# Kernel optimization log

Hardware: AMD Instinct MI355X
Metric: run time of the kernel (lower is better)

## Reference

```python
import jax, jax.numpy as jnp
import numpy as np

DIMS = 2048
HEADS = 16
HEAD_DIM = DIMS // HEADS  # 128
WIN = 256
THETA = 10000.0


def rotate_half(x):
    x1, x2 = jnp.split(x, 2, axis=-1)
    return jnp.concatenate([-x2, x1], axis=-1)


def rope_freqs(seq_len):
    inv_freq = 1.0 / (THETA ** (jnp.arange(0, HEAD_DIM, 2, dtype=jnp.float32) / HEAD_DIM))
    f = jnp.outer(jnp.arange(seq_len, dtype=jnp.float32), inv_freq)  # [S, D/2]
    return jnp.concatenate([f, f], axis=-1)[None, :, None, :]  # [1, S, 1, D]


def setup_inputs() -> dict:
    key = jax.random.key(0)
    ks = jax.random.split(key, 5)
    B, S = 2, 8192
    scale = 1.0 / np.sqrt(DIMS).astype(np.float32)
    return {
        "hidden_states": jax.random.normal(ks[0], (B, S, DIMS), jnp.float32),
        "Wq": jax.random.normal(ks[1], (DIMS, DIMS), jnp.float32) * scale,
        "Wk": jax.random.normal(ks[2], (DIMS, DIMS), jnp.float32) * scale,
        "Wv": jax.random.normal(ks[3], (DIMS, DIMS), jnp.float32) * scale,
        "Wo": jax.random.normal(ks[4], (DIMS, DIMS), jnp.float32) * scale,
    }


def reference(hidden_states, Wq, Wk, Wv, Wo):
    B, S, _ = hidden_states.shape
    # projections (weights stored [in, out])
    q = (hidden_states @ Wq).reshape(B, S, HEADS, HEAD_DIM)
    k = (hidden_states @ Wk).reshape(B, S, HEADS, HEAD_DIM)
    v = (hidden_states @ Wv).reshape(B, S, HEADS, HEAD_DIM)

    freqs = rope_freqs(S)
    cos, sin = jnp.cos(freqs), jnp.sin(freqs)
    q = q * cos + rotate_half(q) * sin
    k = k * cos + rotate_half(k) * sin

    C = S // WIN
    qc = q.reshape(B, C, WIN, HEADS, HEAD_DIM)
    kc = k.reshape(B, C, WIN, HEADS, HEAD_DIM)
    vc = v.reshape(B, C, WIN, HEADS, HEAD_DIM)

    # previous chunk's K/V (zeros for chunk 0; masked out anyway)
    kp = jnp.concatenate([jnp.zeros_like(kc[:, :1]), kc[:, :-1]], axis=1)
    vp = jnp.concatenate([jnp.zeros_like(vc[:, :1]), vc[:, :-1]], axis=1)
    kcat = jnp.concatenate([kp, kc], axis=2)  # [B, C, 2W, H, D]
    vcat = jnp.concatenate([vp, vc], axis=2)

    scores = jnp.einsum('bcqhd,bckhd->bchqk', qc, kcat) / np.float32(np.sqrt(HEAD_DIM))

    causal = jnp.tril(jnp.ones((WIN, WIN), dtype=bool))  # current-chunk causal
    prev_ok = (jnp.arange(C) > 0)[:, None, None]  # chunk 0 has no previous chunk
    mask = jnp.concatenate([
        jnp.broadcast_to(prev_ok, (C, WIN, WIN)),
        jnp.broadcast_to(causal[None], (C, WIN, WIN)),
    ], axis=-1)  # [C, W, 2W]

    scores = jnp.where(mask[None, :, None], scores, -jnp.inf)
    probs = jax.nn.softmax(scores, axis=-1)
    out = jnp.einsum('bchqk,bckhd->bcqhd', probs, vcat)
    out = out.reshape(B, S, DIMS)
    return out @ Wo
```

## Files before the change

kernel.cpp:

```cpp
#include <hip/hip_runtime.h>
#include <cmath>

#define DIMS 2048
#define SEQ  8192
#define NB   2
#define HEADS 16
#define HD   128
#define WINW 256
#define MROWS 16384
#define NCH  32

using bf16x8 = __attribute__((ext_vector_type(8))) short;
using f32x4  = __attribute__((ext_vector_type(4))) float;

__device__ __forceinline__ unsigned short f2bf(float f) {
  unsigned int u = __float_as_uint(f);
  u += 0x7FFF + ((u >> 16) & 1);
  return (unsigned short)(u >> 16);
}

__device__ __forceinline__ void async16(const unsigned short* g, unsigned short* l) {
  __builtin_amdgcn_global_load_lds((const __attribute__((address_space(1))) void*)g,
                                   (__attribute__((address_space(3))) void*)l,
                                   16, 0, 0);
}

#define BAR() __builtin_amdgcn_s_barrier()
#define WAIT_LGKM0() do { asm volatile("s_waitcnt lgkmcnt(0)" ::: "memory"); \
                          __builtin_amdgcn_sched_barrier(0); } while (0)
#define WAIT_LGKM(n) do { asm volatile("s_waitcnt lgkmcnt(" #n ")" ::: "memory"); \
                          __builtin_amdgcn_sched_barrier(0); } while (0)
#define ORDER() asm volatile("" ::: "memory")
#define WAIT_VM(n) asm volatile("s_waitcnt vmcnt(" #n ")" ::: "memory")
#define MFMA16(a, b, c) __builtin_amdgcn_mfma_f32_16x16x32_bf16(a, b, c, 0, 0, 0)

__global__ __launch_bounds__(256) void prep(
    const float* __restrict__ w0, const float* __restrict__ w1,
    const float* __restrict__ w2, const float* __restrict__ w3,
    const float* __restrict__ H,
    unsigned short* __restrict__ Wt, unsigned short* __restrict__ Hb,
    float* __restrict__ cosT, float* __restrict__ sinT) {
  __shared__ unsigned short tile[64][65];
  const int bid = blockIdx.x;
  const int t = threadIdx.x;
  if (bid < 4096) {
    const int z = bid & 3;
    const int rest = bid >> 2;
    const int n0 = (rest & 31) * 64, k0 = (rest >> 5) * 64;
    const float* W = (z == 0) ? w0 : (z == 1) ? w1 : (z == 2) ? w2 : w3;
    unsigned short* O = Wt + (size_t)z * DIMS * DIMS;
    #pragma unroll
    for (int p = 0; p < 16; ++p) {
      int i = p * 4 + (t >> 6);
      int j = t & 63;
      tile[i][j] = f2bf(W[(size_t)(k0 + i) * DIMS + n0 + j]);
    }
    __syncthreads();
    #pragma unroll
    for (int p = 0; p < 16; ++p) {
      int a = p * 4 + (t >> 6);
      int b = t & 63;
      O[(size_t)(n0 + a) * DIMS + k0 + b] = tile[b][a];
    }
  } else if (bid < 6144) {
    const long n4 = (long)MROWS * DIMS / 4;
    long i = (long)(bid - 4096) * 256 + t;
    for (; i < n4; i += 524288) {
      float4 v = ((const float4*)H)[i];
      ushort4 o;
      o.x = f2bf(v.x); o.y = f2bf(v.y); o.z = f2bf(v.z); o.w = f2bf(v.w);
      ((ushort4*)Hb)[i] = o;
    }
  } else {
    int tl = (bid - 6144) * 256 + t;
    int pos = tl >> 6, i = tl & 63;
    double inv = pow(10000.0, -(double)i / 64.0);
    double ang = (double)pos * inv;
    cosT[tl] = (float)cos(ang);
    sinT[tl] = (float)sin(ang);
  }
}

template<int MODE>
__global__ __launch_bounds__(512, 2) void gemm256(
    const unsigned short* __restrict__ A,
    const unsigned short* __restrict__ WtAll,
    unsigned short* __restrict__ OutB,
    float* __restrict__ OutF,
    const float* __restrict__ cosT,
    const float* __restrict__ sinT) {
  __shared__ __align__(1024) unsigned short lds[65536];
  unsigned short* const As0 = lds;
  unsigned short* const Bs0 = lds + 16384;
  unsigned short* const As1 = lds + 32768;
  unsigned short* const Bs1 = lds + 49152;

  const int tid = threadIdx.x;
  const int wid = tid >> 6, lane = tid & 63;
  const int lo = lane & 15, hi = lane >> 4;
  const int wm = wid >> 2, wn = wid & 3;
  const int flip = (lo & 7) << 4;

  const int nwg = gridDim.x;
  const int orig = blockIdx.x;
  const int bid = (orig & 7) * (nwg >> 3) + (orig >> 3);

  int by, bx, z;
  if (MODE == 0) {
    z = bid >> 9;
    by = (bid & 511) >> 3;
    bx = bid & 7;
  } else {
    by = bid >> 3; bx = bid & 7; z = 3;
  }
  const int m0 = by * 256, n0 = bx * 256;
  const unsigned short* const Ag = A;
  const unsigned short* const Bg = WtAll + (size_t)z * DIMS * DIMS;

  f32x4 acc[8][4];
  #pragma unroll
  for (int i = 0; i < 8; ++i)
    #pragma unroll
    for (int j = 0; j < 4; ++j)
      acc[i][j] = (f32x4){0.f, 0.f, 0.f, 0.f};

  auto stage_half = [&](const unsigned short* __restrict__ G, int grow0, int tile,
                        unsigned short* dst) {
    const int k0 = tile * 64;
    #pragma unroll
    for (int h8 = 0; h8 < 2; ++h8) {
      const int c = h8 * 8 + wid;
      const int row = c * 8 + (lane >> 3);
      const int col8 = (lane & 7) ^ (lane >> 3);
      async16(G + (size_t)(grow0 + row) * DIMS + k0 + col8 * 8, dst + c * 512);
    }
  };
  auto rdA = [&](const unsigned short* base, int i, int kk) -> bf16x8 {
    const int r = i * 32 + wm * 16 + lo;
    const int cb = (kk * 64 + hi * 16) ^ flip;
    return *(const bf16x8*)((const char*)base + r * 128 + cb);
  };
  auto rdB = [&](const unsigned short* base, int j, int kk) -> bf16x8 {
    const int r = j * 64 + wn * 16 + lo;
    const int cb = (kk * 64 + hi * 16) ^ flip;
    return *(const bf16x8*)((const char*)base + r * 128 + cb);
  };

  bf16x8 aq[4][2], b0[2][2], b1[2][2];

  stage_half(Ag, m0,       0, As0);
  stage_half(Bg, n0,       0, Bs0);
  stage_half(Ag, m0 + 128, 0, As0 + 8192);
  stage_half(Bg, n0 + 128, 0, Bs0 + 8192);
  stage_half(Ag, m0,       1, As1);
  stage_half(Bg, n0,       1, Bs1);
  stage_half(Bg, n0 + 128, 1, Bs1 + 8192);
  WAIT_VM(6);
  BAR();

  #pragma unroll 1
  for (int it = 0; it < 16; ++it) {
    const int t = 2 * it;
    const bool pre = (it < 15);
    #pragma unroll
    for (int i = 0; i < 4; ++i) aq[i][0] = rdA(As0, i, 0);
    #pragma unroll
    for (int j = 0; j < 2; ++j) b0[j][0] = rdB(Bs0, j, 0);
    ORDER();
    #pragma unroll
    for (int i = 0; i < 4; ++i) aq[i][1] = rdA(As0, i, 1);
    #pragma unroll
    for (int j = 0; j < 2; ++j) b0[j][1] = rdB(Bs0, j, 1);
    stage_half(Ag, m0 + 128, t + 1, As1 + 8192);
    WAIT_LGKM(6);
    __builtin_amdgcn_s_setprio(1);
    #pragma unroll
    for (int i = 0; i < 4; ++i)
      #pragma unroll
      for (int j = 0; j < 2; ++j)
        acc[i][j] = MFMA16(aq[i][0], b0[j][0], acc[i][j]);
    WAIT_LGKM0();
    #pragma unroll
    for (int i = 0; i < 4; ++i)
      #pragma unroll
      for (int j = 0; j < 2; ++j)
        acc[i][j] = MFMA16(aq[i][1], b0[j][1], acc[i][j]);
    __builtin_amdgcn_s_setprio(0);
    BAR();
    #pragma unroll
    for (int j = 0; j < 2; ++j) b1[j][0] = rdB(Bs0, 2 + j, 0);
    ORDER();
    #pragma unroll
    for (int j = 0; j < 2; ++j) b1[j][1] = rdB(Bs0, 2 + j, 1);
    if (pre) stage_half(Ag, m0, t + 2, As0);
    WAIT_LGKM(2);
    __builtin_amdgcn_s_setprio(1);
    #pragma unroll
    for (int i = 0; i < 4; ++i)
      #pragma unroll
      for (int j = 0; j < 2; ++j)
        acc[i][2 + j] = MFMA16(aq[i][0], b1[j][0], acc[i][2 + j]);
    WAIT_LGKM0();
    #pragma unroll
    for (int i = 0; i < 4; ++i)
      #pragma unroll
      for (int j = 0; j < 2; ++j)
        acc[i][2 + j] = MFMA16(aq[i][1], b1[j][1], acc[i][2 + j]);
    __builtin_amdgcn_s_setprio(0);
    BAR();
    #pragma unroll
    for (int i = 0; i < 4; ++i) aq[i][0] = rdA(As0, 4 + i, 0);
    ORDER();
    #pragma unroll
    for (int i = 0; i < 4; ++i) aq[i][1] = rdA(As0, 4 + i, 1);
    if (pre) stage_half(Bg, n0, t + 2, Bs0);
    WAIT_LGKM(4);
    __builtin_amdgcn_s_setprio(1);
    #pragma unroll
    for (int i = 0; i < 4; ++i)
      #pragma unroll
      for (int j = 0; j < 2; ++j)
        acc[4 + i][j] = MFMA16(aq[i][0], b0[j][0], acc[4 + i][j]);
    WAIT_LGKM0();
    #pragma unroll
    for (int i = 0; i < 4; ++i)
      #pragma unroll
      for (int j = 0; j < 2; ++j)
        acc[4 + i][j] = MFMA16(aq[i][1], b0[j][1], acc[4 + i][j]);
    __builtin_amdgcn_s_setprio(0);
    BAR();
    if (pre) stage_half(Bg, n0 + 128, t + 2, Bs0 + 8192);
    __builtin_amdgcn_s_setprio(1);
    #pragma unroll
    for (int kk = 0; kk < 2; ++kk)
      #pragma unroll
      for (int i = 0; i < 4; ++i)
        #pragma unroll
        for (int j = 0; j < 2; ++j)
          acc[4 + i][2 + j] = MFMA16(aq[i][kk], b1[j][kk], acc[4 + i][2 + j]);
    __builtin_amdgcn_s_setprio(0);
    if (it == 15) { WAIT_VM(0); } else { WAIT_VM(6); }
    BAR();
    #pragma unroll
    for (int i = 0; i < 4; ++i) aq[i][0] = rdA(As1, i, 0);
    #pragma unroll
    for (int j = 0; j < 2; ++j) b0[j][0] = rdB(Bs1, j, 0);
    ORDER();
    #pragma unroll
    for (int i = 0; i < 4; ++i) aq[i][1] = rdA(As1, i, 1);
    #pragma unroll
    for (int j = 0; j < 2; ++j) b0[j][1] = rdB(Bs1, j, 1);
    if (pre) stage_half(Ag, m0 + 128, t + 2, As0 + 8192);
    WAIT_LGKM(6);
    __builtin_amdgcn_s_setprio(1);
    #pragma unroll
    for (int i = 0; i < 4; ++i)
      #pragma unroll
      for (int j = 0; j < 2; ++j)
        acc[i][j] = MFMA16(aq[i][0], b0[j][0], acc[i][j]);
    WAIT_LGKM0();
    #pragma unroll
    for (int i = 0; i < 4; ++i)
      #pragma unroll
      for (int j = 0; j < 2; ++j)
        acc[i][j] = MFMA16(aq[i][1], b0[j][1], acc[i][j]);
    __builtin_amdgcn_s_setprio(0);
    BAR();
    #pragma unroll
    for (int j = 0; j < 2; ++j) b1[j][0] = rdB(Bs1, 2 + j, 0);
    ORDER();
    #pragma unroll
    for (int j = 0; j < 2; ++j) b1[j][1] = rdB(Bs1, 2 + j, 1);
    if (pre) stage_half(Ag, m0, t + 3, As1);
    WAIT_LGKM(2);
    __builtin_amdgcn_s_setprio(1);
    #pragma unroll
    for (int i = 0; i < 4; ++i)
      #pragma unroll
      for (int j = 0; j < 2; ++j)
        acc[i][2 + j] = MFMA16(aq[i][0], b1[j][0], acc[i][2 + j]);
    WAIT_LGKM0();
    #pragma unroll
    for (int i = 0; i < 4; ++i)
      #pragma unroll
      for (int j = 0; j < 2; ++j)
        acc[i][2 + j] = MFMA16(aq[i][1], b1[j][1], acc[i][2 + j]);
    __builtin_amdgcn_s_setprio(0);
    BAR();
    #pragma unroll
    for (int i = 0; i < 4; ++i) aq[i][0] = rdA(As1, 4 + i, 0);
    ORDER();
    #pragma unroll
    for (int i = 0; i < 4; ++i) aq[i][1] = rdA(As1, 4 + i, 1);
    if (pre) stage_half(Bg, n0, t + 3, Bs1);
    WAIT_LGKM(4);
    __builtin_amdgcn_s_setprio(1);
    #pragma unroll
    for (int i = 0; i < 4; ++i)
      #pragma unroll
      for (int j = 0; j < 2; ++j)
        acc[4 + i][j] = MFMA16(aq[i][0], b0[j][0], acc[4 + i][j]);
    WAIT_LGKM0();
    #pragma unroll
    for (int i = 0; i < 4; ++i)
      #pragma unroll
      for (int j = 0; j < 2; ++j)
        acc[4 + i][j] = MFMA16(aq[i][1], b0[j][1], acc[4 + i][j]);
    __builtin_amdgcn_s_setprio(0);
    BAR();
    if (pre) stage_half(Bg, n0 + 128, t + 3, Bs1 + 8192);
    __builtin_amdgcn_s_setprio(1);
    #pragma unroll
    for (int kk = 0; kk < 2; ++kk)
      #pragma unroll
      for (int i = 0; i < 4; ++i)
        #pragma unroll
        for (int j = 0; j < 2; ++j)
          acc[4 + i][2 + j] = MFMA16(aq[i][kk], b1[j][kk], acc[4 + i][2 + j]);
    __builtin_amdgcn_s_setprio(0);
    WAIT_VM(6);
    BAR();
  }

  if (MODE == 0 && z == 2) {
    unsigned short* vt = OutB + (size_t)2 * MROWS * DIMS;
    #pragma unroll
    for (int i = 0; i < 8; ++i) {
      const int row0 = m0 + i * 32 + wm * 16 + hi * 4;
      const int bb = row0 >> 13;
      const int s0 = row0 & (SEQ - 1);
      #pragma unroll
      for (int j = 0; j < 4; ++j) {
        const int colg = n0 + j * 64 + wn * 16 + lo;
        ushort4 pk;
        pk.x = f2bf(acc[i][j][0]); pk.y = f2bf(acc[i][j][1]);
        pk.z = f2bf(acc[i][j][2]); pk.w = f2bf(acc[i][j][3]);
        *(ushort4*)&vt[(((size_t)(bb * 2048 + colg)) << 13) + s0] = pk;
      }
    }
  } else {
    unsigned short* outb = (MODE == 0) ? (OutB + (size_t)z * MROWS * DIMS)
                                       : (unsigned short*)nullptr;
    #pragma unroll
    for (int i = 0; i < 8; ++i) {
      #pragma unroll
      for (int rr = 0; rr < 4; ++rr) {
        const int row = m0 + i * 32 + wm * 16 + hi * 4 + rr;
        const int s = row & (SEQ - 1);
        if (MODE == 1) {
          float* o = OutF + (size_t)row * DIMS + n0;
          #pragma unroll
          for (int j = 0; j < 4; ++j) o[j * 64 + wn * 16 + lo] = acc[i][j][rr];
        } else {
          unsigned short* o = outb + (size_t)row * DIMS + n0;
          const int d = wn * 16 + lo;
          const float cc = cosT[s * 64 + d], sn = sinT[s * 64 + d];
          #pragma unroll
          for (int p = 0; p < 2; ++p) {
            const float v1 = acc[i][2 * p][rr], v2 = acc[i][2 * p + 1][rr];
            o[p * 128 + d]      = f2bf(v1 * cc - v2 * sn);
            o[p * 128 + d + 64] = f2bf(v2 * cc + v1 * sn);
          }
        }
      }
    }
  }
}

__global__ __launch_bounds__(256, 2) void attn(
    const unsigned short* __restrict__ Qb,
    const unsigned short* __restrict__ Kb,
    const unsigned short* __restrict__ Vt,
    unsigned short* __restrict__ AO) {
  __shared__ unsigned short Ksm[2][64 * 128];
  __shared__ unsigned short Vsm[2][128 * 64];
  __shared__ unsigned short Psm[4 * 32 * 64];

  const int nwg = gridDim.x;
  const int orig = blockIdx.x;
  const int bid = (orig & 7) * (nwg >> 3) + (orig >> 3);

  const int qh = bid & 1;
  const int h = (bid >> 1) & 15;
  const int c = (bid >> 5) & 31;
  const int b = bid >> 10;
  const int tid = threadIdx.x;
  const int wid = tid >> 6, lane = tid & 63;
  const int lo = lane & 15, hi = lane >> 4;
  const float SCALE = 0.08838834764831845f;

  const int qbase = qh * 128 + wid * 32;

  bf16x8 qf[2][4];
  {
    const size_t base = ((size_t)(b * SEQ + c * WINW + qbase + lo)) * DIMS + h * HD;
    #pragma unroll
    for (int m = 0; m < 2; ++m)
      #pragma unroll
      for (int ks = 0; ks < 4; ++ks)
        qf[m][ks] = *(const bf16x8*)&Qb[base + (size_t)m * 16 * DIMS + ks * 32 + hi * 8];
  }

  f32x4 O[2][8];
  float mrow[2][4], lrow[2][4];
  #pragma unroll
  for (int m = 0; m < 2; ++m) {
    #pragma unroll
    for (int n = 0; n < 8; ++n) O[m][n] = (f32x4){0.f, 0.f, 0.f, 0.f};
    #pragma unroll
    for (int r = 0; r < 4; ++r) { mrow[m][r] = -INFINITY; lrow[m][r] = 0.f; }
  }

  unsigned short* Pw = Psm + wid * 32 * 64;
  const int t0 = (c == 0) ? 4 : 0;
  const int tend = 5 + 2 * qh;

  const unsigned short* Kg0 = Kb + ((size_t)(b * SEQ + (c - 1) * WINW)) * DIMS + h * HD;
  const unsigned short* Vg0 = Vt + (((size_t)(b * 2048 + h * HD)) << 13) + (c - 1) * WINW;

  auto stageKV = [&](int t, int pb) {
    #pragma unroll
    for (int p = 0; p < 4; ++p) {
      const int cid = p * 256 + tid;
      const int row = cid >> 4, c16 = cid & 15;
      async16(Kg0 + (size_t)(t * 64 + row) * DIMS + ((c16 ^ (row & 7)) << 3),
              &Ksm[pb][cid * 8]);
    }
    #pragma unroll
    for (int p = 0; p < 4; ++p) {
      const int cid = p * 256 + tid;
      const int rd = cid >> 3, c8 = cid & 7;
      async16(Vg0 + ((size_t)rd << 13) + t * 64 + ((c8 ^ (rd & 7)) << 3),
              &Vsm[pb][cid * 8]);
    }
  };

  stageKV(t0, t0 & 1);
  for (int t = t0; t <= tend; ++t) {
    const int pb = t & 1;
    if (t < tend) { stageKV(t + 1, pb ^ 1); WAIT_VM(8); } else { WAIT_VM(0); }
    BAR();

    const bool active = (t < 4) || (((t - 4) << 6) <= qbase + 31);
    if (active) {
      f32x4 S[2][4];
      #pragma unroll
      for (int m = 0; m < 2; ++m)
        #pragma unroll
        for (int n = 0; n < 4; ++n)
          S[m][n] = (f32x4){0.f, 0.f, 0.f, 0.f};
      const char* Kbase = (const char*)&Ksm[pb][0];
      #pragma unroll
      for (int ks = 0; ks < 4; ++ks) {
        bf16x8 kf[4];
        #pragma unroll
        for (int n = 0; n < 4; ++n)
          kf[n] = *(const bf16x8*)(Kbase + (n * 16 + lo) * 256 +
                                   (((ks * 4 + hi) ^ (lo & 7)) << 4));
        #pragma unroll
        for (int m = 0; m < 2; ++m)
          #pragma unroll
          for (int n = 0; n < 4; ++n)
            S[m][n] = MFMA16(qf[m][ks], kf[n], S[m][n]);
      }

      float tmax[2][4];
      #pragma unroll
      for (int m = 0; m < 2; ++m) {
        #pragma unroll
        for (int r = 0; r < 4; ++r) {
          const int qrow = qbase + m * 16 + hi * 4 + r;
          float tm = -INFINITY;
          #pragma unroll
          for (int n = 0; n < 4; ++n) {
            const int kc = t * 64 + n * 16 + lo;
            float v = S[m][n][r] * SCALE;
            const bool ok = (kc < WINW) ? (c > 0) : ((kc - WINW) <= qrow);
            v = ok ? v : -INFINITY;
            S[m][n][r] = v;
            tm = fmaxf(tm, v);
          }
          tm = fmaxf(tm, __shfl_xor(tm, 1));
          tm = fmaxf(tm, __shfl_xor(tm, 2));
          tm = fmaxf(tm, __shfl_xor(tm, 4));
          tm = fmaxf(tm, __shfl_xor(tm, 8));
          tmax[m][r] = tm;
        }
      }
      float need = -INFINITY;
      #pragma unroll
      for (int m = 0; m < 2; ++m)
        #pragma unroll
        for (int r = 0; r < 4; ++r)
          need = fmaxf(need, tmax[m][r] - mrow[m][r]);
      const bool fast = __all(need <= 8.0f);

      #pragma unroll
      for (int m = 0; m < 2; ++m) {
        #pragma unroll
        for (int r = 0; r < 4; ++r) {
          float mused = mrow[m][r];
          if (!fast) {
            mused = fmaxf(mused, tmax[m][r]);
            const float corr = __expf(mrow[m][r] - mused);
            lrow[m][r] *= corr;
            #pragma unroll
            for (int n = 0; n < 8; ++n) O[m][n][r] *= corr;
            mrow[m][r] = mused;
          }
          float rsum = 0.f;
          #pragma unroll
          for (int n = 0; n < 4; ++n) {
            const float p = __expf(S[m][n][r] - mused);
            S[m][n][r] = p;
            rsum += p;
          }
          rsum += __shfl_xor(rsum, 1);
          rsum += __shfl_xor(rsum, 2);
          rsum += __shfl_xor(rsum, 4);
          rsum += __shfl_xor(rsum, 8);
          lrow[m][r] += rsum;
          const int q = m * 16 + hi * 4 + r;
          #pragma unroll
          for (int n = 0; n < 4; ++n) {
            const int boff = (q << 7) + (((n * 16 + lo) << 1) ^ ((q & 7) << 4));
            *(unsigned short*)((char*)Pw + boff) = f2bf(S[m][n][r]);
          }
        }
      }
      asm volatile("" ::: "memory");

      const char* Vbase = (const char*)&Vsm[pb][0];
      #pragma unroll
      for (int kk = 0; kk < 2; ++kk) {
        bf16x8 pf[2], vf[8];
        #pragma unroll
        for (int m = 0; m < 2; ++m) {
          const int q = m * 16 + lo;
          pf[m] = *(const bf16x8*)((const char*)Pw + (q << 7) +
                                   (((kk * 4 + hi) << 4) ^ ((q & 7) << 4)));
        }
        #pragma unroll
        for (int n = 0; n < 8; ++n)
          vf[n] = *(const bf16x8*)(Vbase + (n * 16 + lo) * 128 +
                                   (((kk * 4 + hi) ^ (lo & 7)) << 4));
        #pragma unroll
        for (int m = 0; m < 2; ++m)
          #pragma unroll
          for (int n = 0; n < 8; ++n)
            O[m][n] = MFMA16(pf[m], vf[n], O[m][n]);
      }
    }
    BAR();
  }

  #pragma unroll
  for (int m = 0; m < 2; ++m) {
    #pragma unroll
    for (int r = 0; r < 4; ++r) {
      const float inv = 1.f / lrow[m][r];
      const size_t row = (size_t)(b * SEQ + c * WINW + qbase + m * 16 + hi * 4 + r);
      unsigned short* o = AO + row * DIMS + h * HD;
      #pragma unroll
      for (int n = 0; n < 8; ++n)
        o[n * 16 + lo] = f2bf(O[m][n][r] * inv);
    }
  }
}

extern "C" void kernel_launch(void* const* d_in, const int* in_sizes, int n_in,
                              void* d_out, int out_size, void* d_ws, size_t ws_size,
                              hipStream_t stream) {
  const float* H  = (const float*)d_in[0];
  const float* Wq = (const float*)d_in[1];
  const float* Wk = (const float*)d_in[2];
  const float* Wv = (const float*)d_in[3];
  const float* Wo = (const float*)d_in[4];
  float* out = (float*)d_out;

  unsigned short* Wt  = (unsigned short*)d_ws;
  unsigned short* Hb  = Wt + (size_t)4 * DIMS * DIMS;
  unsigned short* QKV = Hb + (size_t)MROWS * DIMS;
  unsigned short* AO  = QKV + (size_t)3 * MROWS * DIMS;
  float* cosT = (float*)(AO + (size_t)MROWS * DIMS);
  float* sinT = cosT + (size_t)SEQ * 64;

  prep<<<8192, 256, 0, stream>>>(Wq, Wk, Wv, Wo, H, Wt, Hb, cosT, sinT);
  gemm256<0><<<1536, 512, 0, stream>>>(Hb, Wt, QKV, nullptr, cosT, sinT);
  attn<<<2048, 256, 0, stream>>>(QKV, QKV + (size_t)MROWS * DIMS,
                                 QKV + (size_t)2 * MROWS * DIMS, AO);
  gemm256<1><<<512, 512, 0, stream>>>(AO, Wt, nullptr, out, cosT, sinT);
}
```

Before: 707.4 us.

## Merge GEMM quadrant phases into two per stage to halve barriers

Restructures the 256x256 GEMM main loop so each LDS stage runs two phases (top-half rows, bottom-half rows) that each load all four B column groups, instead of four quadrant phases. The number of block barriers and waitcnt points per k-step drops. Global-to-LDS staging for the next tile is bunched into one phase, and the wait counts are adjusted. The trade-off is higher register pressure from holding b0 and b1 together, burstier global loads, and less interleaving of memory traffic with MFMA work.

```diff
diff --git a/kernel.cpp b/kernel.cpp
--- a/kernel.cpp
+++ b/kernel.cpp
@@ -162,161 +162,125 @@
   for (int it = 0; it < 16; ++it) {
     const int t = 2 * it;
     const bool pre = (it < 15);
+
     #pragma unroll
     for (int i = 0; i < 4; ++i) aq[i][0] = rdA(As0, i, 0);
     #pragma unroll
-    for (int j = 0; j < 2; ++j) b0[j][0] = rdB(Bs0, j, 0);
+    for (int j = 0; j < 2; ++j) { b0[j][0] = rdB(Bs0, j, 0); b1[j][0] = rdB(Bs0, 2 + j, 0); }
     ORDER();
     #pragma unroll
     for (int i = 0; i < 4; ++i) aq[i][1] = rdA(As0, i, 1);
     #pragma unroll
-    for (int j = 0; j < 2; ++j) b0[j][1] = rdB(Bs0, j, 1);
+    for (int j = 0; j < 2; ++j) { b0[j][1] = rdB(Bs0, j, 1); b1[j][1] = rdB(Bs0, 2 + j, 1); }
     stage_half(Ag, m0 + 128, t + 1, As1 + 8192);
-    WAIT_LGKM(6);
+    WAIT_LGKM(8);
     __builtin_amdgcn_s_setprio(1);
     #pragma unroll
     for (int i = 0; i < 4; ++i)
       #pragma unroll
-      for (int j = 0; j < 2; ++j)
-        acc[i][j] = MFMA16(aq[i][0], b0[j][0], acc[i][j]);
+      for (int j = 0; j < 2; ++j) {
+        acc[i][j]     = MFMA16(aq[i][0], b0[j][0], acc[i][j]);
+        acc[i][2 + j] = MFMA16(aq[i][0], b1[j][0], acc[i][2 + j]);
+      }
     WAIT_LGKM0();
     #pragma unroll
     for (int i = 0; i < 4; ++i)
       #pragma unroll
-      for (int j = 0; j < 2; ++j)
-        acc[i][j] = MFMA16(aq[i][1], b0[j][1], acc[i][j]);
+      for (int j = 0; j < 2; ++j) {
+        acc[i][j]     = MFMA16(aq[i][1], b0[j][1], acc[i][j]);
+        acc[i][2 + j] = MFMA16(aq[i][1], b1[j][1], acc[i][2 + j]);
+      }
     __builtin_amdgcn_s_setprio(0);
     BAR();
-    #pragma unroll
-    for (int j = 0; j < 2; ++j) b1[j][0] = rdB(Bs0, 2 + j, 0);
-    ORDER();
-    #pragma unroll
-    for (int j = 0; j < 2; ++j) b1[j][1] = rdB(Bs0, 2 + j, 1);
-    if (pre) stage_half(Ag, m0, t + 2, As0);
-    WAIT_LGKM(2);
-    __builtin_amdgcn_s_setprio(1);
-    #pragma unroll
-    for (int i = 0; i < 4; ++i)
-      #pragma unroll
-      for (int j = 0; j < 2; ++j)
-        acc[i][2 + j] = MFMA16(aq[i][0], b1[j][0], acc[i][2 + j]);
-    WAIT_LGKM0();
-    #pragma unroll
-    for (int i = 0; i < 4; ++i)
-      #pragma unroll
-      for (int j = 0; j < 2; ++j)
-        acc[i][2 + j] = MFMA16(aq[i][1], b1[j][1], acc[i][2 + j]);
-    __builtin_amdgcn_s_setprio(0);
-    BAR();
+
     #pragma unroll
     for (int i = 0; i < 4; ++i) aq[i][0] = rdA(As0, 4 + i, 0);
     ORDER();
     #pragma unroll
     for (int i = 0; i < 4; ++i) aq[i][1] = rdA(As0, 4 + i, 1);
-    if (pre) stage_half(Bg, n0, t + 2, Bs0);
+    if (pre) {
+      stage_half(Ag, m0,       t + 2, As0);
+      stage_half(Bg, n0,       t + 2, Bs0);
+      stage_half(Bg, n0 + 128, t + 2, Bs0 + 8192);
+    }
     WAIT_LGKM(4);
     __builtin_amdgcn_s_setprio(1);
     #pragma unroll
     for (int i = 0; i < 4; ++i)
       #pragma unroll
-      for (int j = 0; j < 2; ++j)
-        acc[4 + i][j] = MFMA16(aq[i][0], b0[j][0], acc[4 + i][j]);
+      for (int j = 0; j < 2; ++j) {
+        acc[4 + i][j]     = MFMA16(aq[i][0], b0[j][0], acc[4 + i][j]);
+        acc[4 + i][2 + j] = MFMA16(aq[i][0], b1[j][0], acc[4 + i][2 + j]);
+      }
     WAIT_LGKM0();
     #pragma unroll
     for (int i = 0; i < 4; ++i)
       #pragma unroll
-      for (int j = 0; j < 2; ++j)
-        acc[4 + i][j] = MFMA16(aq[i][1], b0[j][1], acc[4 + i][j]);
-    __builtin_amdgcn_s_setprio(0);
-    BAR();
-    if (pre) stage_half(Bg, n0 + 128, t + 2, Bs0 + 8192);
-    __builtin_amdgcn_s_setprio(1);
-    #pragma unroll
-    for (int kk = 0; kk < 2; ++kk)
-      #pragma unroll
-      for (int i = 0; i < 4; ++i)
-        #pragma unroll
-        for (int j = 0; j < 2; ++j)
-          acc[4 + i][2 + j] = MFMA16(aq[i][kk], b1[j][kk], acc[4 + i][2 + j]);
+      for (int j = 0; j < 2; ++j) {
+        acc[4 + i][j]     = MFMA16(aq[i][1], b0[j][1], acc[4 + i][j]);
+        acc[4 + i][2 + j] = MFMA16(aq[i][1], b1[j][1], acc[4 + i][2 + j]);
+      }
     __builtin_amdgcn_s_setprio(0);
     if (it == 15) { WAIT_VM(0); } else { WAIT_VM(6); }
     BAR();
+
     #pragma unroll
     for (int i = 0; i < 4; ++i) aq[i][0] = rdA(As1, i, 0);
     #pragma unroll
-    for (int j = 0; j < 2; ++j) b0[j][0] = rdB(Bs1, j, 0);
+    for (int j = 0; j < 2; ++j) { b0[j][0] = rdB(Bs1, j, 0); b1[j][0] = rdB(Bs1, 2 + j, 0); }
     ORDER();
     #pragma unroll
     for (int i = 0; i < 4; ++i) aq[i][1] = rdA(As1, i, 1);
     #pragma unroll
-    for (int j = 0; j < 2; ++j) b0[j][1] = rdB(Bs1, j, 1);
+    for (int j = 0; j < 2; ++j) { b0[j][1] = rdB(Bs1, j, 1); b1[j][1] = rdB(Bs1, 2 + j, 1); }
     if (pre) stage_half(Ag, m0 + 128, t + 2, As0 + 8192);
-    WAIT_LGKM(6);
+    WAIT_LGKM(8);
     __builtin_amdgcn_s_setprio(1);
     #pragma unroll
     for (int i = 0; i < 4; ++i)
       #pragma unroll
-      for (int j = 0; j < 2; ++j)
-        acc[i][j] = MFMA16(aq[i][0], b0[j][0], acc[i][j]);
+      for (int j = 0; j < 2; ++j) {
+        acc[i][j]     = MFMA16(aq[i][0], b0[j][0], acc[i][j]);
+        acc[i][2 + j] = MFMA16(aq[i][0], b1[j][0], acc[i][2 + j]);
+      }
     WAIT_LGKM0();
     #pragma unroll
     for (int i = 0; i < 4; ++i)
       #pragma unroll
-      for (int j = 0; j < 2; ++j)
-        acc[i][j] = MFMA16(aq[i][1], b0[j][1], acc[i][j]);
+      for (int j = 0; j < 2; ++j) {
+        acc[i][j]     = MFMA16(aq[i][1], b0[j][1], acc[i][j]);
+        acc[i][2 + j] = MFMA16(aq[i][1], b1[j][1], acc[i][2 + j]);
+      }
     __builtin_amdgcn_s_setprio(0);
     BAR();
-    #pragma unroll
-    for (int j = 0; j < 2; ++j) b1[j][0] = rdB(Bs1, 2 + j, 0);
-    ORDER();
-    #pragma unroll
-    for (int j = 0; j < 2; ++j) b1[j][1] = rdB(Bs1, 2 + j, 1);
-    if (pre) stage_half(Ag, m0, t + 3, As1);
-    WAIT_LGKM(2);
-    __builtin_amdgcn_s_setprio(1);
-    #pragma unroll
-    for (int i = 0; i < 4; ++i)
-      #pragma unroll
-      for (int j = 0; j < 2; ++j)
-        acc[i][2 + j] = MFMA16(aq[i][0], b1[j][0], acc[i][2 + j]);
-    WAIT_LGKM0();
-    #pragma unroll
-    for (int i = 0; i < 4; ++i)
-      #pragma unroll
-      for (int j = 0; j < 2; ++j)
-        acc[i][2 + j] = MFMA16(aq[i][1], b1[j][1], acc[i][2 + j]);
-    __builtin_amdgcn_s_setprio(0);
-    BAR();
+
     #pragma unroll
     for (int i = 0; i < 4; ++i) aq[i][0] = rdA(As1, 4 + i, 0);
     ORDER();
     #pragma unroll
     for (int i = 0; i < 4; ++i) aq[i][1] = rdA(As1, 4 + i, 1);
-    if (pre) stage_half(Bg, n0, t + 3, Bs1);
+    if (pre) {
+      stage_half(Ag, m0,       t + 3, As1);
+      stage_half(Bg, n0,       t + 3, Bs1);
+      stage_half(Bg, n0 + 128, t + 3, Bs1 + 8192);
+    }
     WAIT_LGKM(4);
     __builtin_amdgcn_s_setprio(1);
     #pragma unroll
     for (int i = 0; i < 4; ++i)
       #pragma unroll
-      for (int j = 0; j < 2; ++j)
-        acc[4 + i][j] = MFMA16(aq[i][0], b0[j][0], acc[4 + i][j]);
+      for (int j = 0; j < 2; ++j) {
+        acc[4 + i][j]     = MFMA16(aq[i][0], b0[j][0], acc[4 + i][j]);
+        acc[4 + i][2 + j] = MFMA16(aq[i][0], b1[j][0], acc[4 + i][2 + j]);
+      }
     WAIT_LGKM0();
     #pragma unroll
     for (int i = 0; i < 4; ++i)
       #pragma unroll
-      for (int j = 0; j < 2; ++j)
-        acc[4 + i][j] = MFMA16(aq[i][1], b0[j][1], acc[4 + i][j]);
-    __builtin_amdgcn_s_setprio(0);
-    BAR();
-    if (pre) stage_half(Bg, n0 + 128, t + 3, Bs1 + 8192);
-    __builtin_amdgcn_s_setprio(1);
-    #pragma unroll
-    for (int kk = 0; kk < 2; ++kk)
-      #pragma unroll
-      for (int i = 0; i < 4; ++i)
-        #pragma unroll
-        for (int j = 0; j < 2; ++j)
-          acc[4 + i][2 + j] = MFMA16(aq[i][kk], b1[j][kk], acc[4 + i][2 + j]);
+      for (int j = 0; j < 2; ++j) {
+        acc[4 + i][j]     = MFMA16(aq[i][1], b0[j][1], acc[4 + i][j]);
+        acc[4 + i][2 + j] = MFMA16(aq[i][1], b1[j][1], acc[4 + i][2 + j]);
+      }
     __builtin_amdgcn_s_setprio(0);
     WAIT_VM(6);
     BAR();
```

After: 719.9 us. Within noise of the previous version (+1.8%).
